# Optimization experiments

Measured on AMD Instinct MI355X. Metric: run time of the kernel, lower is better.

Reference implementation:

```python
import jax, jax.numpy as jnp
import numpy as np

N_SENT = 262144
N_BAGS = 4096
HIDDEN = 256
HIER = 2
LAYER0 = 14
NUM_CLASSES = 53


def setup_inputs() -> dict:
    key = jax.random.key(0)
    ks = jax.random.split(key, 8)
    x = jax.random.normal(ks[0], (N_SENT, HIDDEN), dtype=jnp.float32)
    rel_emb0 = jax.random.normal(ks[1], (LAYER0, HIDDEN), dtype=jnp.float32) * 0.1
    rel_emb1 = jax.random.normal(ks[2], (NUM_CLASSES, HIDDEN), dtype=jnp.float32) * 0.1
    disc = jax.random.normal(ks[3], (NUM_CLASSES, 2 * HIDDEN), dtype=jnp.float32) * 0.05
    bias = jnp.zeros((NUM_CLASSES,), dtype=jnp.float32)
    # relation_levels[r] = (coarse node id, fine node id) for relation r
    relation_levels = jnp.stack(
        [jax.random.randint(ks[4], (NUM_CLASSES,), 0, LAYER0, dtype=jnp.int32),
         jnp.arange(NUM_CLASSES, dtype=jnp.int32)], axis=1)
    label_index = jax.random.randint(ks[5], (N_SENT,), 0, NUM_CLASSES, dtype=jnp.int32)
    # ragged bag boundaries: scope[0]=0, scope[-1]=N_SENT, interior sorted
    interior = jnp.sort(jax.random.randint(ks[6], (N_BAGS - 1,), 1, N_SENT, dtype=jnp.int32))
    scope = jnp.concatenate([jnp.zeros((1,), jnp.int32), interior,
                             jnp.full((1,), N_SENT, jnp.int32)])
    return {"x": x, "rel_emb0": rel_emb0, "rel_emb1": rel_emb1, "disc": disc,
            "bias": bias, "relation_levels": relation_levels,
            "label_index": label_index, "scope": scope}


def _segment_ids(scope, n):
    # scope: [B+1] sorted boundaries -> per-sentence bag id [n]
    marks = jnp.zeros((n,), jnp.int32).at[scope[1:-1]].add(1)
    return jnp.cumsum(marks)


def reference(x, rel_emb0, rel_emb1, disc, bias, relation_levels, label_index, scope):
    n = x.shape[0]
    b = scope.shape[0] - 1
    seg = _segment_ids(scope, n)                       # [N]
    ll = relation_levels[label_index]                  # [N, 2]
    # per-level attention logits: <rel_emb[level][node], x>
    lg0 = jnp.sum(rel_emb0[ll[:, 0]] * x, axis=-1)     # [N]
    lg1 = jnp.sum(rel_emb1[ll[:, 1]] * x, axis=-1)     # [N]
    logits = jnp.stack([lg0, lg1], axis=1)             # [N, hier]
    # ragged softmax per bag (stable)
    m = jax.ops.segment_max(logits, seg, num_segments=b)     # [B, hier]
    e = jnp.exp(logits - m[seg])
    s = jax.ops.segment_sum(e, seg, num_segments=b)          # [B, hier]
    score = e / s[seg]                                       # [N, hier]
    # attention-weighted sentence reduction per bag per level
    weighted = score[:, :, None] * x[:, None, :]             # [N, hier, H]
    repre = jax.ops.segment_sum(weighted, seg, num_segments=b)  # [B, hier, H]
    stack_repre = repre.reshape(b, HIER * HIDDEN)            # [B, 2H]
    return stack_repre @ disc.T + bias                       # [B, 53]
```

## Files before the change

kernel.cpp:

```cpp
#include <hip/hip_runtime.h>
#include <math.h>

#define HIDDEN 256
#define NUM_CLASSES 53
#define NWAVES 4
#define BLOCK (NWAVES * 64)

__global__ __launch_bounds__(BLOCK, 8) void hattn_fused_kernel(
    const float* __restrict__ x,
    const float* __restrict__ rel_emb0,
    const float* __restrict__ rel_emb1,
    const float* __restrict__ disc,
    const float* __restrict__ bias,
    const int* __restrict__ relation_levels,
    const int* __restrict__ label_index,
    const int* __restrict__ scope,
    float* __restrict__ out)
{
    const int bag   = blockIdx.x;
    const int start = scope[bag];
    const int end   = scope[bag + 1];

    const int tid  = threadIdx.x;
    const int lane = tid & 63;
    const int wave = tid >> 6;
    const int col  = lane * 4;

    float m0 = -INFINITY, m1 = -INFINITY;
    float l0 = 0.f, l1 = 0.f;
    float4 o0 = make_float4(0.f, 0.f, 0.f, 0.f);
    float4 o1 = make_float4(0.f, 0.f, 0.f, 0.f);

    for (int s = start + wave; s < end; s += NWAVES * 2) {
        const int s2   = s + NWAVES;
        const bool has2 = (s2 < end);
        const int s2c  = has2 ? s2 : s;

        const float4 xa = *reinterpret_cast<const float4*>(x + (size_t)s  * HIDDEN + col);
        const float4 xb = *reinterpret_cast<const float4*>(x + (size_t)s2c * HIDDEN + col);
        const int lbl_a = label_index[s];
        const int lbl_b = label_index[s2c];
        const int ca0 = relation_levels[2 * lbl_a];
        const int ca1 = relation_levels[2 * lbl_a + 1];
        const int cb0 = relation_levels[2 * lbl_b];
        const int cb1 = relation_levels[2 * lbl_b + 1];

        const float4 ra0 = *reinterpret_cast<const float4*>(rel_emb0 + ca0 * HIDDEN + col);
        const float4 ra1 = *reinterpret_cast<const float4*>(rel_emb1 + ca1 * HIDDEN + col);
        const float4 rb0 = *reinterpret_cast<const float4*>(rel_emb0 + cb0 * HIDDEN + col);
        const float4 rb1 = *reinterpret_cast<const float4*>(rel_emb1 + cb1 * HIDDEN + col);

        float pa0 = xa.x * ra0.x + xa.y * ra0.y + xa.z * ra0.z + xa.w * ra0.w;
        float pa1 = xa.x * ra1.x + xa.y * ra1.y + xa.z * ra1.z + xa.w * ra1.w;
        float pb0 = xb.x * rb0.x + xb.y * rb0.y + xb.z * rb0.z + xb.w * rb0.w;
        float pb1 = xb.x * rb1.x + xb.y * rb1.y + xb.z * rb1.z + xb.w * rb1.w;

        #pragma unroll
        for (int off = 32; off > 0; off >>= 1) {
            pa0 += __shfl_xor(pa0, off, 64);
            pa1 += __shfl_xor(pa1, off, 64);
            pb0 += __shfl_xor(pb0, off, 64);
            pb1 += __shfl_xor(pb1, off, 64);
        }

        {
            const float mx  = has2 ? fmaxf(pa0, pb0) : pa0;
            const float nm  = fmaxf(m0, mx);
            const float al  = __expf(m0 - nm);
            const float ea  = __expf(pa0 - nm);
            const float eb  = has2 ? __expf(pb0 - nm) : 0.f;
            l0 = l0 * al + ea + eb;
            o0.x = o0.x * al + ea * xa.x + eb * xb.x;
            o0.y = o0.y * al + ea * xa.y + eb * xb.y;
            o0.z = o0.z * al + ea * xa.z + eb * xb.z;
            o0.w = o0.w * al + ea * xa.w + eb * xb.w;
            m0 = nm;
        }
        {
            const float mx  = has2 ? fmaxf(pa1, pb1) : pa1;
            const float nm  = fmaxf(m1, mx);
            const float al  = __expf(m1 - nm);
            const float ea  = __expf(pa1 - nm);
            const float eb  = has2 ? __expf(pb1 - nm) : 0.f;
            l1 = l1 * al + ea + eb;
            o1.x = o1.x * al + ea * xa.x + eb * xb.x;
            o1.y = o1.y * al + ea * xa.y + eb * xb.y;
            o1.z = o1.z * al + ea * xa.z + eb * xb.z;
            o1.w = o1.w * al + ea * xa.w + eb * xb.w;
            m1 = nm;
        }
    }

    __shared__ float s_m[NWAVES][2];
    __shared__ float s_l[NWAVES][2];
    __shared__ float s_o[2][NWAVES][HIDDEN];
    __shared__ float s_repre[2 * HIDDEN];

    if (lane == 0) {
        s_m[wave][0] = m0; s_m[wave][1] = m1;
        s_l[wave][0] = l0; s_l[wave][1] = l1;
    }
    *reinterpret_cast<float4*>(&s_o[0][wave][col]) = o0;
    *reinterpret_cast<float4*>(&s_o[1][wave][col]) = o1;
    __syncthreads();

    {
        const int t = tid;
        #pragma unroll
        for (int h = 0; h < 2; ++h) {
            float M = -INFINITY;
            #pragma unroll
            for (int w = 0; w < NWAVES; ++w) M = fmaxf(M, s_m[w][h]);
            float L = 0.f, acc = 0.f;
            #pragma unroll
            for (int w = 0; w < NWAVES; ++w) {
                const float mw = s_m[w][h];
                const float f  = (mw == -INFINITY) ? 0.f : __expf(mw - M);
                L   += s_l[w][h] * f;
                acc += s_o[h][w][t] * f;
            }
            const float inv = (L > 0.f) ? (1.f / L) : 0.f;
            s_repre[h * HIDDEN + t] = acc * inv;
        }
    }
    __syncthreads();

    for (int c = wave; c < NUM_CLASSES; c += NWAVES) {
        const float* dr = disc + c * (2 * HIDDEN);
        float p = 0.f;
        #pragma unroll
        for (int k = 0; k < 8; ++k) {
            const int j = lane + k * 64;
            p += s_repre[j] * dr[j];
        }
        #pragma unroll
        for (int off = 32; off > 0; off >>= 1)
            p += __shfl_xor(p, off, 64);
        if (lane == 0)
            out[bag * NUM_CLASSES + c] = p + bias[c];
    }
}

extern "C" void kernel_launch(void* const* d_in, const int* in_sizes, int n_in,
                              void* d_out, int out_size, void* d_ws, size_t ws_size,
                              hipStream_t stream) {
    const float* x               = (const float*)d_in[0];
    const float* rel_emb0        = (const float*)d_in[1];
    const float* rel_emb1        = (const float*)d_in[2];
    const float* disc            = (const float*)d_in[3];
    const float* bias            = (const float*)d_in[4];
    const int*   relation_levels = (const int*)d_in[5];
    const int*   label_index     = (const int*)d_in[6];
    const int*   scope           = (const int*)d_in[7];
    float*       out             = (float*)d_out;

    const int n_bags = in_sizes[7] - 1;

    hattn_fused_kernel<<<n_bags, BLOCK, 0, stream>>>(
        x, rel_emb0, rel_emb1, disc, bias, relation_levels, label_index, scope, out);
}
```

Baseline: 455.7 us.

## Split wavefront into half-waves per row and batch four rows per iteration

Each wave now handles two sentence rows at once, with each half-wave loading eight floats per lane. The loop batches four such row pairs per iteration, so more independent global loads are in flight and the online-softmax rescale runs once per batch. Dot-product reductions need one fewer shuffle step. The cost is more registers and a lower launch-bounds occupancy hint (4 instead of 8), plus a larger shared-memory merge across eight partial states.

```diff
diff --git a/kernel.cpp b/kernel.cpp
--- a/kernel.cpp
+++ b/kernel.cpp
@@ -5,8 +5,9 @@
 #define NUM_CLASSES 53
 #define NWAVES 4
 #define BLOCK (NWAVES * 64)
+#define KP 4
 
-__global__ __launch_bounds__(BLOCK, 8) void hattn_fused_kernel(
+__global__ __launch_bounds__(BLOCK, 4) void hattn_fused_kernel(
     const float* __restrict__ x,
     const float* __restrict__ rel_emb0,
     const float* __restrict__ rel_emb1,
@@ -24,84 +25,117 @@
     const int tid  = threadIdx.x;
     const int lane = tid & 63;
     const int wave = tid >> 6;
-    const int col  = lane * 4;
+    const int half = lane >> 5;
+    const int j    = lane & 31;
+    const int colb = j * 8;
 
-    float m0 = -INFINITY, m1 = -INFINITY;
-    float l0 = 0.f, l1 = 0.f;
-    float4 o0 = make_float4(0.f, 0.f, 0.f, 0.f);
-    float4 o1 = make_float4(0.f, 0.f, 0.f, 0.f);
+    float m0 = -INFINITY, l0 = 0.f;
+    float m1 = -INFINITY, l1 = 0.f;
+    float4 o0a = make_float4(0,0,0,0), o0b = make_float4(0,0,0,0);
+    float4 o1a = make_float4(0,0,0,0), o1b = make_float4(0,0,0,0);
 
-    for (int s = start + wave; s < end; s += NWAVES * 2) {
-        const int s2   = s + NWAVES;
-        const bool has2 = (s2 < end);
-        const int s2c  = has2 ? s2 : s;
-
-        const float4 xa = *reinterpret_cast<const float4*>(x + (size_t)s  * HIDDEN + col);
-        const float4 xb = *reinterpret_cast<const float4*>(x + (size_t)s2c * HIDDEN + col);
-        const int lbl_a = label_index[s];
-        const int lbl_b = label_index[s2c];
-        const int ca0 = relation_levels[2 * lbl_a];
-        const int ca1 = relation_levels[2 * lbl_a + 1];
-        const int cb0 = relation_levels[2 * lbl_b];
-        const int cb1 = relation_levels[2 * lbl_b + 1];
-
-        const float4 ra0 = *reinterpret_cast<const float4*>(rel_emb0 + ca0 * HIDDEN + col);
-        const float4 ra1 = *reinterpret_cast<const float4*>(rel_emb1 + ca1 * HIDDEN + col);
-        const float4 rb0 = *reinterpret_cast<const float4*>(rel_emb0 + cb0 * HIDDEN + col);
-        const float4 rb1 = *reinterpret_cast<const float4*>(rel_emb1 + cb1 * HIDDEN + col);
-
-        float pa0 = xa.x * ra0.x + xa.y * ra0.y + xa.z * ra0.z + xa.w * ra0.w;
-        float pa1 = xa.x * ra1.x + xa.y * ra1.y + xa.z * ra1.z + xa.w * ra1.w;
-        float pb0 = xb.x * rb0.x + xb.y * rb0.y + xb.z * rb0.z + xb.w * rb0.w;
-        float pb1 = xb.x * rb1.x + xb.y * rb1.y + xb.z * rb1.z + xb.w * rb1.w;
+    for (int base = start + 2 * wave; base < end; base += 2 * NWAVES * KP) {
+        float4 fa[KP], fb[KP];
+        int2   rl[KP];
+        bool   val[KP];
 
         #pragma unroll
-        for (int off = 32; off > 0; off >>= 1) {
-            pa0 += __shfl_xor(pa0, off, 64);
-            pa1 += __shfl_xor(pa1, off, 64);
-            pb0 += __shfl_xor(pb0, off, 64);
-            pb1 += __shfl_xor(pb1, off, 64);
+        for (int k = 0; k < KP; ++k) {
+            const int a  = base + 2 * NWAVES * k;
+            const int r  = a + half;
+            const bool v = (r < end);
+            const int rc = v ? r : start;
+            val[k] = v;
+            const float* xp = x + (size_t)rc * HIDDEN + colb;
+            fa[k] = *reinterpret_cast<const float4*>(xp);
+            fb[k] = *reinterpret_cast<const float4*>(xp + 4);
+            const int lbl = label_index[rc];
+            rl[k] = *reinterpret_cast<const int2*>(relation_levels + 2 * lbl);
+        }
+
+        float lg0[KP], lg1[KP];
+        #pragma unroll
+        for (int k = 0; k < KP; ++k) {
+            const float* p0 = rel_emb0 + (size_t)rl[k].x * HIDDEN + colb;
+            const float* p1 = rel_emb1 + (size_t)rl[k].y * HIDDEN + colb;
+            const float4 r0a = *reinterpret_cast<const float4*>(p0);
+            const float4 r0b = *reinterpret_cast<const float4*>(p0 + 4);
+            const float4 r1a = *reinterpret_cast<const float4*>(p1);
+            const float4 r1b = *reinterpret_cast<const float4*>(p1 + 4);
+
+            float pa0 = fa[k].x*r0a.x + fa[k].y*r0a.y + fa[k].z*r0a.z + fa[k].w*r0a.w
+                      + fb[k].x*r0b.x + fb[k].y*r0b.y + fb[k].z*r0b.z + fb[k].w*r0b.w;
+            float pa1 = fa[k].x*r1a.x + fa[k].y*r1a.y + fa[k].z*r1a.z + fa[k].w*r1a.w
+                      + fb[k].x*r1b.x + fb[k].y*r1b.y + fb[k].z*r1b.z + fb[k].w*r1b.w;
+
+            #pragma unroll
+            for (int off = 16; off > 0; off >>= 1) {
+                pa0 += __shfl_xor(pa0, off, 64);
+                pa1 += __shfl_xor(pa1, off, 64);
+            }
+            lg0[k] = val[k] ? pa0 : -INFINITY;
+            lg1[k] = val[k] ? pa1 : -INFINITY;
         }
 
         {
-            const float mx  = has2 ? fmaxf(pa0, pb0) : pa0;
-            const float nm  = fmaxf(m0, mx);
-            const float al  = __expf(m0 - nm);
-            const float ea  = __expf(pa0 - nm);
-            const float eb  = has2 ? __expf(pb0 - nm) : 0.f;
-            l0 = l0 * al + ea + eb;
-            o0.x = o0.x * al + ea * xa.x + eb * xb.x;
-            o0.y = o0.y * al + ea * xa.y + eb * xb.y;
-            o0.z = o0.z * al + ea * xa.z + eb * xb.z;
-            o0.w = o0.w * al + ea * xa.w + eb * xb.w;
+            float bm = fmaxf(fmaxf(lg0[0], lg0[1]), fmaxf(lg0[2], lg0[3]));
+            const float nm = fmaxf(m0, bm);
+            const float al = (m0 == -INFINITY) ? 0.f : __expf(m0 - nm);
+            float e[KP], se = 0.f;
+            #pragma unroll
+            for (int k = 0; k < KP; ++k) {
+                e[k] = (lg0[k] == -INFINITY) ? 0.f : __expf(lg0[k] - nm);
+                se += e[k];
+            }
+            l0 = l0 * al + se;
+            o0a.x = o0a.x*al + e[0]*fa[0].x + e[1]*fa[1].x + e[2]*fa[2].x + e[3]*fa[3].x;
+            o0a.y = o0a.y*al + e[0]*fa[0].y + e[1]*fa[1].y + e[2]*fa[2].y + e[3]*fa[3].y;
+            o0a.z = o0a.z*al + e[0]*fa[0].z + e[1]*fa[1].z + e[2]*fa[2].z + e[3]*fa[3].z;
+            o0a.w = o0a.w*al + e[0]*fa[0].w + e[1]*fa[1].w + e[2]*fa[2].w + e[3]*fa[3].w;
+            o0b.x = o0b.x*al + e[0]*fb[0].x + e[1]*fb[1].x + e[2]*fb[2].x + e[3]*fb[3].x;
+            o0b.y = o0b.y*al + e[0]*fb[0].y + e[1]*fb[1].y + e[2]*fb[2].y + e[3]*fb[3].y;
+            o0b.z = o0b.z*al + e[0]*fb[0].z + e[1]*fb[1].z + e[2]*fb[2].z + e[3]*fb[3].z;
+            o0b.w = o0b.w*al + e[0]*fb[0].w + e[1]*fb[1].w + e[2]*fb[2].w + e[3]*fb[3].w;
             m0 = nm;
         }
         {
-            const float mx  = has2 ? fmaxf(pa1, pb1) : pa1;
-            const float nm  = fmaxf(m1, mx);
-            const float al  = __expf(m1 - nm);
-            const float ea  = __expf(pa1 - nm);
-            const float eb  = has2 ? __expf(pb1 - nm) : 0.f;
-            l1 = l1 * al + ea + eb;
-            o1.x = o1.x * al + ea * xa.x + eb * xb.x;
-            o1.y = o1.y * al + ea * xa.y + eb * xb.y;
-            o1.z = o1.z * al + ea * xa.z + eb * xb.z;
-            o1.w = o1.w * al + ea * xa.w + eb * xb.w;
+            float bm = fmaxf(fmaxf(lg1[0], lg1[1]), fmaxf(lg1[2], lg1[3]));
+            const float nm = fmaxf(m1, bm);
+            const float al = (m1 == -INFINITY) ? 0.f : __expf(m1 - nm);
+            float e[KP], se = 0.f;
+            #pragma unroll
+            for (int k = 0; k < KP; ++k) {
+                e[k] = (lg1[k] == -INFINITY) ? 0.f : __expf(lg1[k] - nm);
+                se += e[k];
+            }
+            l1 = l1 * al + se;
+            o1a.x = o1a.x*al + e[0]*fa[0].x + e[1]*fa[1].x + e[2]*fa[2].x + e[3]*fa[3].x;
+            o1a.y = o1a.y*al + e[0]*fa[0].y + e[1]*fa[1].y + e[2]*fa[2].y + e[3]*fa[3].y;
+            o1a.z = o1a.z*al + e[0]*fa[0].z + e[1]*fa[1].z + e[2]*fa[2].z + e[3]*fa[3].z;
+            o1a.w = o1a.w*al + e[0]*fa[0].w + e[1]*fa[1].w + e[2]*fa[2].w + e[3]*fa[3].w;
+            o1b.x = o1b.x*al + e[0]*fb[0].x + e[1]*fb[1].x + e[2]*fb[2].x + e[3]*fb[3].x;
+            o1b.y = o1b.y*al + e[0]*fb[0].y + e[1]*fb[1].y + e[2]*fb[2].y + e[3]*fb[3].y;
+            o1b.z = o1b.z*al + e[0]*fb[0].z + e[1]*fb[1].z + e[2]*fb[2].z + e[3]*fb[3].z;
+            o1b.w = o1b.w*al + e[0]*fb[0].w + e[1]*fb[1].w + e[2]*fb[2].w + e[3]*fb[3].w;
             m1 = nm;
         }
     }
 
-    __shared__ float s_m[NWAVES][2];
-    __shared__ float s_l[NWAVES][2];
-    __shared__ float s_o[2][NWAVES][HIDDEN];
+    __shared__ float s_m[NWAVES][2][2];
+    __shared__ float s_l[NWAVES][2][2];
+    __shared__ float s_o[2][NWAVES][2][HIDDEN];
     __shared__ float s_repre[2 * HIDDEN];
 
-    if (lane == 0) {
-        s_m[wave][0] = m0; s_m[wave][1] = m1;
-        s_l[wave][0] = l0; s_l[wave][1] = l1;
+    if (j == 0) {
+        s_m[wave][half][0] = m0;  s_m[wave][half][1] = m1;
+        s_l[wave][half][0] = l0;  s_l[wave][half][1] = l1;
     }
-    *reinterpret_cast<float4*>(&s_o[0][wave][col]) = o0;
-    *reinterpret_cast<float4*>(&s_o[1][wave][col]) = o1;
+    {
+        float4* d0 = reinterpret_cast<float4*>(&s_o[0][wave][half][colb]);
+        d0[0] = o0a; d0[1] = o0b;
+        float4* d1 = reinterpret_cast<float4*>(&s_o[1][wave][half][colb]);
+        d1[0] = o1a; d1[1] = o1b;
+    }
     __syncthreads();
 
     {
@@ -110,17 +144,21 @@
         for (int h = 0; h < 2; ++h) {
             float M = -INFINITY;
             #pragma unroll
-            for (int w = 0; w < NWAVES; ++w) M = fmaxf(M, s_m[w][h]);
+            for (int w = 0; w < NWAVES; ++w)
+                #pragma unroll
+                for (int hh = 0; hh < 2; ++hh)
+                    M = fmaxf(M, s_m[w][hh][h]);
             float L = 0.f, acc = 0.f;
             #pragma unroll
-            for (int w = 0; w < NWAVES; ++w) {
-                const float mw = s_m[w][h];
-                const float f  = (mw == -INFINITY) ? 0.f : __expf(mw - M);
-                L   += s_l[w][h] * f;
-                acc += s_o[h][w][t] * f;
-            }
-            const float inv = (L > 0.f) ? (1.f / L) : 0.f;
-            s_repre[h * HIDDEN + t] = acc * inv;
+            for (int w = 0; w < NWAVES; ++w)
+                #pragma unroll
+                for (int hh = 0; hh < 2; ++hh) {
+                    const float mw = s_m[w][hh][h];
+                    const float f  = (mw == -INFINITY) ? 0.f : __expf(mw - M);
+                    L   += s_l[w][hh][h] * f;
+                    acc += s_o[h][w][hh][t] * f;
+                }
+            s_repre[h * HIDDEN + t] = (L > 0.f) ? (acc / L) : 0.f;
         }
     }
     __syncthreads();
@@ -130,8 +168,8 @@
         float p = 0.f;
         #pragma unroll
         for (int k = 0; k < 8; ++k) {
-            const int j = lane + k * 64;
-            p += s_repre[j] * dr[j];
+            const int idx = lane + k * 64;
+            p += s_repre[idx] * dr[idx];
         }
         #pragma unroll
         for (int off = 32; off > 0; off >>= 1)
```

Measured after the change: 430.2 us. -5.6%, faster.

## Split fused bag attention into segment, logits and weighted-sum kernels

Applied to the files above, without the earlier changes.

Replaces the single per-bag fused online-softmax kernel with three kernels. The first writes a per-row segment id, the second computes exp-logits in fixed row chunks and accumulates per-bag sums with shared and global atomics, and the third does the normalized weighted reduction and classifier per bag. The goal is to balance load across ragged bags and to drop the online max/rescale work. In exchange x is read twice, which adds memory traffic. The softmax also drops max subtraction, so large logits can overflow.

```diff
diff --git a/kernel.cpp b/kernel.cpp
--- a/kernel.cpp
+++ b/kernel.cpp
@@ -3,17 +3,104 @@
 
 #define HIDDEN 256
 #define NUM_CLASSES 53
-#define NWAVES 4
-#define BLOCK (NWAVES * 64)
-
-__global__ __launch_bounds__(BLOCK, 8) void hattn_fused_kernel(
+#define CHUNK 64
+#define CAP 66
+
+__global__ __launch_bounds__(256) void k0_seg(
+    const int* __restrict__ scope, int* __restrict__ seg,
+    float* __restrict__ s, int n_bags)
+{
+    const int gtid = blockIdx.x * blockDim.x + threadIdx.x;
+    if (gtid < 2 * n_bags) s[gtid] = 0.f;
+    const int wid  = gtid >> 6;
+    const int lane = gtid & 63;
+    if (wid < n_bags) {
+        const int st = scope[wid], en = scope[wid + 1];
+        for (int i = st + lane; i < en; i += 64) seg[i] = wid;
+    }
+}
+
+__global__ __launch_bounds__(256) void k1_logits(
     const float* __restrict__ x,
     const float* __restrict__ rel_emb0,
     const float* __restrict__ rel_emb1,
+    const int* __restrict__ relation_levels,
+    const int* __restrict__ label_index,
+    const int* __restrict__ seg,
+    float* __restrict__ e,
+    float* __restrict__ s)
+{
+    const int c0   = blockIdx.x * CHUNK;
+    const int tid  = threadIdx.x;
+    const int lane = tid & 63;
+    const int wave = tid >> 6;
+    const int half = lane >> 5;
+    const int j    = lane & 31;
+    const int colb = j * 8;
+    const int stream = wave * 2 + half;
+
+    __shared__ float s_local[2 * CAP];
+    __shared__ int   s_seg0;
+    if (tid == 0) s_seg0 = seg[c0];
+    for (int t = tid; t < 2 * CAP; t += 256) s_local[t] = 0.f;
+    __syncthreads();
+    const int seg0 = s_seg0;
+
+    #pragma unroll
+    for (int k = 0; k < CHUNK / 8; ++k) {
+        const int row = c0 + 8 * k + stream;
+        const float* xp = x + (size_t)row * HIDDEN + colb;
+        const float4 xa = *reinterpret_cast<const float4*>(xp);
+        const float4 xb = *reinterpret_cast<const float4*>(xp + 4);
+        const int lbl = label_index[row];
+        const int2 rl = *reinterpret_cast<const int2*>(relation_levels + 2 * lbl);
+        const float* p0 = rel_emb0 + (size_t)rl.x * HIDDEN + colb;
+        const float* p1 = rel_emb1 + (size_t)rl.y * HIDDEN + colb;
+        const float4 r0a = *reinterpret_cast<const float4*>(p0);
+        const float4 r0b = *reinterpret_cast<const float4*>(p0 + 4);
+        const float4 r1a = *reinterpret_cast<const float4*>(p1);
+        const float4 r1b = *reinterpret_cast<const float4*>(p1 + 4);
+
+        float lg0 = xa.x*r0a.x + xa.y*r0a.y + xa.z*r0a.z + xa.w*r0a.w
+                  + xb.x*r0b.x + xb.y*r0b.y + xb.z*r0b.z + xb.w*r0b.w;
+        float lg1 = xa.x*r1a.x + xa.y*r1a.y + xa.z*r1a.z + xa.w*r1a.w
+                  + xb.x*r1b.x + xb.y*r1b.y + xb.z*r1b.z + xb.w*r1b.w;
+
+        #pragma unroll
+        for (int off = 16; off > 0; off >>= 1) {
+            lg0 += __shfl_xor(lg0, off, 64);
+            lg1 += __shfl_xor(lg1, off, 64);
+        }
+
+        if (j == 0) {
+            const float e0 = __expf(lg0);
+            const float e1 = __expf(lg1);
+            e[2 * row]     = e0;
+            e[2 * row + 1] = e1;
+            const int sg = seg[row];
+            const int lb = sg - seg0;
+            if (lb < CAP) {
+                atomicAdd(&s_local[2 * lb],     e0);
+                atomicAdd(&s_local[2 * lb + 1], e1);
+            } else {
+                atomicAdd(&s[2 * sg],     e0);
+                atomicAdd(&s[2 * sg + 1], e1);
+            }
+        }
+    }
+    __syncthreads();
+    for (int t = tid; t < 2 * CAP; t += 256) {
+        const float v = s_local[t];
+        if (v != 0.f) atomicAdd(&s[2 * seg0 + t], v);
+    }
+}
+
+__global__ __launch_bounds__(256) void k2_weighted(
+    const float* __restrict__ x,
+    const float* __restrict__ e,
+    const float* __restrict__ s,
     const float* __restrict__ disc,
     const float* __restrict__ bias,
-    const int* __restrict__ relation_levels,
-    const int* __restrict__ label_index,
     const int* __restrict__ scope,
     float* __restrict__ out)
 {
@@ -24,114 +111,74 @@
     const int tid  = threadIdx.x;
     const int lane = tid & 63;
     const int wave = tid >> 6;
-    const int col  = lane * 4;
-
-    float m0 = -INFINITY, m1 = -INFINITY;
-    float l0 = 0.f, l1 = 0.f;
-    float4 o0 = make_float4(0.f, 0.f, 0.f, 0.f);
-    float4 o1 = make_float4(0.f, 0.f, 0.f, 0.f);
-
-    for (int s = start + wave; s < end; s += NWAVES * 2) {
-        const int s2   = s + NWAVES;
-        const bool has2 = (s2 < end);
-        const int s2c  = has2 ? s2 : s;
-
-        const float4 xa = *reinterpret_cast<const float4*>(x + (size_t)s  * HIDDEN + col);
-        const float4 xb = *reinterpret_cast<const float4*>(x + (size_t)s2c * HIDDEN + col);
-        const int lbl_a = label_index[s];
-        const int lbl_b = label_index[s2c];
-        const int ca0 = relation_levels[2 * lbl_a];
-        const int ca1 = relation_levels[2 * lbl_a + 1];
-        const int cb0 = relation_levels[2 * lbl_b];
-        const int cb1 = relation_levels[2 * lbl_b + 1];
-
-        const float4 ra0 = *reinterpret_cast<const float4*>(rel_emb0 + ca0 * HIDDEN + col);
-        const float4 ra1 = *reinterpret_cast<const float4*>(rel_emb1 + ca1 * HIDDEN + col);
-        const float4 rb0 = *reinterpret_cast<const float4*>(rel_emb0 + cb0 * HIDDEN + col);
-        const float4 rb1 = *reinterpret_cast<const float4*>(rel_emb1 + cb1 * HIDDEN + col);
-
-        float pa0 = xa.x * ra0.x + xa.y * ra0.y + xa.z * ra0.z + xa.w * ra0.w;
-        float pa1 = xa.x * ra1.x + xa.y * ra1.y + xa.z * ra1.z + xa.w * ra1.w;
-        float pb0 = xb.x * rb0.x + xb.y * rb0.y + xb.z * rb0.z + xb.w * rb0.w;
-        float pb1 = xb.x * rb1.x + xb.y * rb1.y + xb.z * rb1.z + xb.w * rb1.w;
-
-        #pragma unroll
-        for (int off = 32; off > 0; off >>= 1) {
-            pa0 += __shfl_xor(pa0, off, 64);
-            pa1 += __shfl_xor(pa1, off, 64);
-            pb0 += __shfl_xor(pb0, off, 64);
-            pb1 += __shfl_xor(pb1, off, 64);
-        }
-
-        {
-            const float mx  = has2 ? fmaxf(pa0, pb0) : pa0;
-            const float nm  = fmaxf(m0, mx);
-            const float al  = __expf(m0 - nm);
-            const float ea  = __expf(pa0 - nm);
-            const float eb  = has2 ? __expf(pb0 - nm) : 0.f;
-            l0 = l0 * al + ea + eb;
-            o0.x = o0.x * al + ea * xa.x + eb * xb.x;
-            o0.y = o0.y * al + ea * xa.y + eb * xb.y;
-            o0.z = o0.z * al + ea * xa.z + eb * xb.z;
-            o0.w = o0.w * al + ea * xa.w + eb * xb.w;
-            m0 = nm;
-        }
-        {
-            const float mx  = has2 ? fmaxf(pa1, pb1) : pa1;
-            const float nm  = fmaxf(m1, mx);
-            const float al  = __expf(m1 - nm);
-            const float ea  = __expf(pa1 - nm);
-            const float eb  = has2 ? __expf(pb1 - nm) : 0.f;
-            l1 = l1 * al + ea + eb;
-            o1.x = o1.x * al + ea * xa.x + eb * xb.x;
-            o1.y = o1.y * al + ea * xa.y + eb * xb.y;
-            o1.z = o1.z * al + ea * xa.z + eb * xb.z;
-            o1.w = o1.w * al + ea * xa.w + eb * xb.w;
-            m1 = nm;
-        }
-    }
-
-    __shared__ float s_m[NWAVES][2];
-    __shared__ float s_l[NWAVES][2];
-    __shared__ float s_o[2][NWAVES][HIDDEN];
+    const int half = lane >> 5;
+    const int j    = lane & 31;
+    const int colb = j * 8;
+    const int stream = wave * 2 + half;
+
+    const float sv0 = s[2 * bag], sv1 = s[2 * bag + 1];
+    const float i0 = (end > start) ? 1.f / sv0 : 0.f;
+    const float i1 = (end > start) ? 1.f / sv1 : 0.f;
+
+    float4 a0 = make_float4(0,0,0,0), b0 = make_float4(0,0,0,0);
+    float4 a1 = make_float4(0,0,0,0), b1 = make_float4(0,0,0,0);
+
+    for (int r = start + stream; r < end; r += 16) {
+        const int r2  = r + 8;
+        const bool v2 = (r2 < end);
+        const int r2c = v2 ? r2 : r;
+
+        const float2 ew1 = *reinterpret_cast<const float2*>(e + 2 * r);
+        const float2 ew2 = *reinterpret_cast<const float2*>(e + 2 * r2c);
+        const float* xp1 = x + (size_t)r   * HIDDEN + colb;
+        const float* xp2 = x + (size_t)r2c * HIDDEN + colb;
+        const float4 x1a = *reinterpret_cast<const float4*>(xp1);
+        const float4 x1b = *reinterpret_cast<const float4*>(xp1 + 4);
+        const float4 x2a = *reinterpret_cast<const float4*>(xp2);
+        const float4 x2b = *reinterpret_cast<const float4*>(xp2 + 4);
+
+        const float w10 = ew1.x * i0, w11 = ew1.y * i1;
+        const float w20 = v2 ? ew2.x * i0 : 0.f;
+        const float w21 = v2 ? ew2.y * i1 : 0.f;
+
+        a0.x += w10*x1a.x + w20*x2a.x;  a0.y += w10*x1a.y + w20*x2a.y;
+        a0.z += w10*x1a.z + w20*x2a.z;  a0.w += w10*x1a.w + w20*x2a.w;
+        b0.x += w10*x1b.x + w20*x2b.x;  b0.y += w10*x1b.y + w20*x2b.y;
+        b0.z += w10*x1b.z + w20*x2b.z;  b0.w += w10*x1b.w + w20*x2b.w;
+        a1.x += w11*x1a.x + w21*x2a.x;  a1.y += w11*x1a.y + w21*x2a.y;
+        a1.z += w11*x1a.z + w21*x2a.z;  a1.w += w11*x1a.w + w21*x2a.w;
+        b1.x += w11*x1b.x + w21*x2b.x;  b1.y += w11*x1b.y + w21*x2b.y;
+        b1.z += w11*x1b.z + w21*x2b.z;  b1.w += w11*x1b.w + w21*x2b.w;
+    }
+
+    __shared__ float s_o[2][8][HIDDEN];
     __shared__ float s_repre[2 * HIDDEN];
-
-    if (lane == 0) {
-        s_m[wave][0] = m0; s_m[wave][1] = m1;
-        s_l[wave][0] = l0; s_l[wave][1] = l1;
-    }
-    *reinterpret_cast<float4*>(&s_o[0][wave][col]) = o0;
-    *reinterpret_cast<float4*>(&s_o[1][wave][col]) = o1;
-    __syncthreads();
-
+    {
+        float4* d0 = reinterpret_cast<float4*>(&s_o[0][stream][colb]);
+        d0[0] = a0; d0[1] = b0;
+        float4* d1 = reinterpret_cast<float4*>(&s_o[1][stream][colb]);
+        d1[0] = a1; d1[1] = b1;
+    }
+    __syncthreads();
     {
         const int t = tid;
         #pragma unroll
         for (int h = 0; h < 2; ++h) {
-            float M = -INFINITY;
+            float acc = 0.f;
             #pragma unroll
-            for (int w = 0; w < NWAVES; ++w) M = fmaxf(M, s_m[w][h]);
-            float L = 0.f, acc = 0.f;
-            #pragma unroll
-            for (int w = 0; w < NWAVES; ++w) {
-                const float mw = s_m[w][h];
-                const float f  = (mw == -INFINITY) ? 0.f : __expf(mw - M);
-                L   += s_l[w][h] * f;
-                acc += s_o[h][w][t] * f;
-            }
-            const float inv = (L > 0.f) ? (1.f / L) : 0.f;
-            s_repre[h * HIDDEN + t] = acc * inv;
-        }
-    }
-    __syncthreads();
-
-    for (int c = wave; c < NUM_CLASSES; c += NWAVES) {
+            for (int w = 0; w < 8; ++w) acc += s_o[h][w][t];
+            s_repre[h * HIDDEN + t] = acc;
+        }
+    }
+    __syncthreads();
+
+    for (int c = wave; c < NUM_CLASSES; c += 4) {
         const float* dr = disc + c * (2 * HIDDEN);
         float p = 0.f;
         #pragma unroll
         for (int k = 0; k < 8; ++k) {
-            const int j = lane + k * 64;
-            p += s_repre[j] * dr[j];
+            const int idx = lane + k * 64;
+            p += s_repre[idx] * dr[idx];
         }
         #pragma unroll
         for (int off = 32; off > 0; off >>= 1)
@@ -155,7 +202,19 @@
     float*       out             = (float*)d_out;
 
     const int n_bags = in_sizes[7] - 1;
-
-    hattn_fused_kernel<<<n_bags, BLOCK, 0, stream>>>(
-        x, rel_emb0, rel_emb1, disc, bias, relation_levels, label_index, scope, out);
-}
+    const int n_rows = in_sizes[6];
+
+    float* s_ws  = (float*)d_ws;
+    float* e_ws  = s_ws + 2 * n_bags;
+    int*   seg   = (int*)(e_ws + 2 * (size_t)n_rows);
+
+    {
+        const int waves  = n_bags;
+        const int blocks = (waves * 64 + 255) / 256;
+        k0_seg<<<blocks, 256, 0, stream>>>(scope, seg, s_ws, n_bags);
+    }
+    k1_logits<<<n_rows / CHUNK, 256, 0, stream>>>(
+        x, rel_emb0, rel_emb1, relation_levels, label_index, seg, e_ws, s_ws);
+    k2_weighted<<<n_bags, 256, 0, stream>>>(
+        x, e_ws, s_ws, disc, bias, scope, out);
+}
```

After: 446.8 us. 1.02x faster.
